# Kernel optimization log

Hardware: AMD Instinct MI355X
Metric: run time of the kernel (lower is better)

Reference implementation:

```python
import jax, jax.numpy as jnp
import numpy as np

EMB = 1024
HEADS = 16
HEAD_DIM = EMB // HEADS
DFF = 4 * EMB
EPS = 1e-5


def setup_inputs() -> dict:
    key = jax.random.key(0)
    ks = jax.random.split(key, 16)
    s = 0.02
    return {
        "x": jax.random.normal(ks[0], (4, 2048, EMB), dtype=jnp.float32),
        "Wq_w": jax.random.normal(ks[1], (EMB, EMB), jnp.float32) * s,
        "Wq_b": jnp.zeros((EMB,), jnp.float32),
        "Wk_w": jax.random.normal(ks[2], (EMB, EMB), jnp.float32) * s,
        "Wk_b": jnp.zeros((EMB,), jnp.float32),
        "Wv_w": jax.random.normal(ks[3], (EMB, EMB), jnp.float32) * s,
        "Wv_b": jnp.zeros((EMB,), jnp.float32),
        "Wo_w": jax.random.normal(ks[4], (EMB, EMB), jnp.float32) * s,
        "Wo_b": jnp.zeros((EMB,), jnp.float32),
        "l1_w": jax.random.normal(ks[5], (DFF, EMB), jnp.float32) * s,
        "l1_b": jnp.zeros((DFF,), jnp.float32),
        "l2_w": jax.random.normal(ks[6], (EMB, DFF), jnp.float32) * s,
        "l2_b": jnp.zeros((EMB,), jnp.float32),
        "n1_scale": jnp.ones((EMB,), jnp.float32),
        "n1_shift": jnp.zeros((EMB,), jnp.float32),
        "n2_scale": jnp.ones((EMB,), jnp.float32),
        "n2_shift": jnp.zeros((EMB,), jnp.float32),
    }


def _layernorm(x, scale, shift):
    # Faithful to the source: mean over last dim, but var over the WHOLE
    # tensor (torch.var with no dim), and divides by var (not std), eps added after.
    mean = jnp.mean(x, axis=-1, keepdims=True)
    var = jnp.var(x)  # scalar, correction=0
    x_norm = (x - mean) / var + EPS
    return x_norm * scale + shift


def _block_forward(x, Wq_w, Wq_b, Wk_w, Wk_b, Wv_w, Wv_b, Wo_w, Wo_b,
                   l1_w, l1_b, l2_w, l2_b, n1_scale, n1_shift, n2_scale, n2_shift):
    B, T, C = x.shape
    shortcut = x
    h = _layernorm(x, n1_scale, n1_shift)

    def proj(w, b):
        y = jnp.einsum('btc,oc->bto', h, w) + b
        return y.reshape(B, T, HEADS, HEAD_DIM).transpose(0, 2, 1, 3)  # bhtd

    q = proj(Wq_w, Wq_b)
    k = proj(Wk_w, Wk_b)
    v = proj(Wv_w, Wv_b)

    scores = jnp.einsum('bhtd,bhsd->bhts', q, k)
    causal = jnp.triu(jnp.ones((T, T), dtype=bool), 1)
    scores = jnp.where(causal, -jnp.inf, scores)
    weights = jax.nn.softmax(scores / jnp.sqrt(jnp.float32(HEAD_DIM)), axis=-1)
    ctx = jnp.einsum('bhts,bhsd->bhtd', weights, v)
    ctx = ctx.transpose(0, 2, 1, 3).reshape(B, T, C)
    attn_out = jnp.einsum('btc,oc->bto', ctx, Wo_w) + Wo_b

    x = attn_out + shortcut
    shortcut = x
    h = _layernorm(x, n2_scale, n2_shift)
    h = jnp.einsum('btc,fc->btf', h, l1_w) + l1_b
    h = jax.nn.gelu(h, approximate=False)
    h = jnp.einsum('btf,cf->btc', h, l2_w) + l2_b
    return h + shortcut


def reference(x, Wq_w, Wq_b, Wk_w, Wk_b, Wv_w, Wv_b, Wo_w, Wo_b,
              l1_w, l1_b, l2_w, l2_b, n1_scale, n1_shift, n2_scale, n2_shift):
    return _block_forward(x, Wq_w, Wq_b, Wk_w, Wk_b, Wv_w, Wv_b, Wo_w, Wo_b,
                          l1_w, l1_b, l2_w, l2_b, n1_scale, n1_shift, n2_scale, n2_shift)
```

## Files before the change

### kernel.cpp

```cpp
#include <hip/hip_runtime.h>
#include <cstdint>

#define EMB   1024
#define HEADS 16
#define HDIM  64
#define DFF   4096
#define TLEN  2048
#define BATCH 4
#define SEQB  8192
#define EPSLN 1e-5f

typedef __attribute__((ext_vector_type(8))) short bf16x8;
typedef __attribute__((ext_vector_type(4))) float f32x4;

#define MFMA16(a, b, c) __builtin_amdgcn_mfma_f32_16x16x32_bf16((a), (b), (c), 0, 0, 0)

__device__ __forceinline__ unsigned short f2bf(float f) {
  unsigned int u = __float_as_uint(f);
  u += 0x7fffu + ((u >> 16) & 1u);
  return (unsigned short)(u >> 16);
}

__device__ __forceinline__ float gelu_f(float x) {
  float x2 = x * x;
  float inner = x * (0.79788456f + 0.035677408f * x2);
  float t = exp2f(2.885390082f * inner);
  return x * t / (t + 1.0f);
}

__global__ __launch_bounds__(256) void cvt_bf16(const float* __restrict__ in,
                                                unsigned short* __restrict__ out, int n4) {
  int i = blockIdx.x * 256 + threadIdx.x;
  if (i >= n4) return;
  float4 v = ((const float4*)in)[i];
  ushort4 o;
  o.x = f2bf(v.x); o.y = f2bf(v.y); o.z = f2bf(v.z); o.w = f2bf(v.w);
  ((ushort4*)out)[i] = o;
}

__global__ __launch_bounds__(256) void pack3(const float* __restrict__ a,
                                             const float* __restrict__ b,
                                             const float* __restrict__ c,
                                             float* __restrict__ o) {
  int i = blockIdx.x * 256 + threadIdx.x;
  o[i] = i < 1024 ? a[i] : (i < 2048 ? b[i - 1024] : c[i - 2048]);
}

__global__ __launch_bounds__(256) void row_reduce(const float* __restrict__ X,
                                                  float* __restrict__ rs,
                                                  float* __restrict__ rq) {
  const int row = blockIdx.x;
  const int tid = threadIdx.x;
  float4 v = ((const float4*)(X + (long)row * EMB))[tid];
  float s = v.x + v.y + v.z + v.w;
  float q = v.x * v.x + v.y * v.y + v.z * v.z + v.w * v.w;
#pragma unroll
  for (int d = 1; d < 64; d <<= 1) { s += __shfl_xor(s, d); q += __shfl_xor(q, d); }
  __shared__ float ss[4], sq[4];
  const int wv = tid >> 6;
  if ((tid & 63) == 0) { ss[wv] = s; sq[wv] = q; }
  __syncthreads();
  if (tid == 0) {
    rs[row] = ss[0] + ss[1] + ss[2] + ss[3];
    rq[row] = sq[0] + sq[1] + sq[2] + sq[3];
  }
}

__global__ __launch_bounds__(256) void finalize_stats(const float* __restrict__ rs,
                                                      const float* __restrict__ rq,
                                                      float* __restrict__ stats) {
  const int tid = threadIdx.x;
  float s = 0.f, q = 0.f;
  for (int i = tid; i < SEQB; i += 256) { s += rs[i]; q += rq[i]; }
#pragma unroll
  for (int d = 1; d < 64; d <<= 1) { s += __shfl_xor(s, d); q += __shfl_xor(q, d); }
  __shared__ float ss[4], sq[4];
  const int wv = tid >> 6;
  if ((tid & 63) == 0) { ss[wv] = s; sq[wv] = q; }
  __syncthreads();
  if (tid == 0) {
    double n = (double)SEQB * (double)EMB;
    double mean = (double)(ss[0] + ss[1] + ss[2] + ss[3]) / n;
    double var = (double)(sq[0] + sq[1] + sq[2] + sq[3]) / n - mean * mean;
    stats[0] = (float)(1.0 / var);
  }
}

__global__ __launch_bounds__(256) void ln_apply(const float* __restrict__ X,
                                                const float* __restrict__ rs,
                                                const float* __restrict__ stats,
                                                const float* __restrict__ scale,
                                                const float* __restrict__ shift,
                                                unsigned short* __restrict__ H) {
  const long i = (long)blockIdx.x * 256 + threadIdx.x;
  const long idx = i * 4;
  const int row = (int)(idx >> 10);
  const int c = (int)(idx & 1023);
  const float mean = rs[row] * (1.0f / EMB);
  const float iv = stats[0];
  float4 x = ((const float4*)X)[i];
  float4 sc = *(const float4*)(scale + c);
  float4 sh = *(const float4*)(shift + c);
  ushort4 o;
  o.x = f2bf(((x.x - mean) * iv + EPSLN) * sc.x + sh.x);
  o.y = f2bf(((x.y - mean) * iv + EPSLN) * sc.y + sh.y);
  o.z = f2bf(((x.z - mean) * iv + EPSLN) * sc.z + sh.z);
  o.w = f2bf(((x.w - mean) * iv + EPSLN) * sc.w + sh.w);
  ((ushort4*)H)[i] = o;
}

template <int EPI>
__global__ __launch_bounds__(256) void gemm_bt(const unsigned short* __restrict__ A,
                                               const unsigned short* __restrict__ W,
                                               const float* __restrict__ bias,
                                               const float* __restrict__ resid,
                                               void* __restrict__ Cout,
                                               unsigned short* __restrict__ kout,
                                               unsigned short* __restrict__ vout,
                                               int M, int N, int K) {
  __shared__ unsigned short sA[128 * 64];
  __shared__ unsigned short sB[128 * 64];
  const int tid = threadIdx.x;
  const int lane = tid & 63;
  const int wave = tid >> 6;
  const int wm = (wave >> 1) * 64, wn = (wave & 1) * 64;
  const int col = lane & 15, quad = lane >> 4;
  const int cx = (col & 7) * 8;

  const int gx = (int)gridDim.x, gy = (int)gridDim.y;
  const int nwg = gx * gy;
  int bid = (int)blockIdx.y * gx + (int)blockIdx.x;
  if ((nwg & 7) == 0) bid = (bid & 7) * (nwg >> 3) + (bid >> 3);
  const int bx = bid % gx;
  const int by = bid / gx;
  const long bm = (long)by * 128, bn = (long)bx * 128;

  f32x4 acc[4][4];
#pragma unroll
  for (int i = 0; i < 4; ++i)
#pragma unroll
    for (int j = 0; j < 4; ++j) acc[i][j] = (f32x4){0.f, 0.f, 0.f, 0.f};

  const int r0 = tid >> 3;
  const int kg = (tid & 7) * 8;
  const int rx = (r0 & 7) * 8;
  const int kgx = kg ^ rx;

  for (int k0 = 0; k0 < K; k0 += 64) {
#pragma unroll
    for (int it = 0; it < 4; ++it) {
      const int r = it * 32 + r0;
      const unsigned short* ga = A + (bm + r) * K + k0 + kgx;
      const unsigned short* gb = W + (bn + r) * K + k0 + kgx;
      __builtin_amdgcn_global_load_lds((const __attribute__((address_space(1))) void*)ga,
                                       (__attribute__((address_space(3))) void*)&sA[r * 64 + kg],
                                       16, 0, 0);
      __builtin_amdgcn_global_load_lds((const __attribute__((address_space(1))) void*)gb,
                                       (__attribute__((address_space(3))) void*)&sB[r * 64 + kg],
                                       16, 0, 0);
    }
    __syncthreads();
#pragma unroll
    for (int ks = 0; ks < 2; ++ks) {
      const int off = (ks * 32 + quad * 8) ^ cx;
      bf16x8 af[4], bfr[4];
#pragma unroll
      for (int mt = 0; mt < 4; ++mt)
        af[mt] = *(const bf16x8*)&sA[(wm + mt * 16 + col) * 64 + off];
#pragma unroll
      for (int nt = 0; nt < 4; ++nt)
        bfr[nt] = *(const bf16x8*)&sB[(wn + nt * 16 + col) * 64 + off];
#pragma unroll
      for (int mt = 0; mt < 4; ++mt)
#pragma unroll
        for (int nt = 0; nt < 4; ++nt) acc[mt][nt] = MFMA16(af[mt], bfr[nt], acc[mt][nt]);
    }
    __syncthreads();
  }

#pragma unroll
  for (int mt = 0; mt < 4; ++mt) {
    const long row0 = bm + wm + mt * 16 + quad * 4;
#pragma unroll
    for (int nt = 0; nt < 4; ++nt) {
      const long c = bn + wn + nt * 16 + col;
      const float bv = bias[c];
      if (EPI == 4) {
        const int seg = (int)(bn >> 10);
        if (seg == 2) {
          ushort4 o;
#pragma unroll
          for (int r = 0; r < 4; ++r) o[r] = f2bf(acc[mt][nt][r] + bv);
          const long bidx = row0 >> 11;
          const long t0 = row0 & 2047;
          *(ushort4*)(vout + (((bidx * 1024 + (c & 1023)) << 11) + t0)) = o;
        } else {
          unsigned short* dst = seg == 0 ? (unsigned short*)Cout : kout;
#pragma unroll
          for (int r = 0; r < 4; ++r)
            dst[(row0 + r) * 1024 + (c & 1023)] = f2bf(acc[mt][nt][r] + bv);
        }
      } else {
#pragma unroll
        for (int r = 0; r < 4; ++r) {
          const long row = row0 + r;
          float v = acc[mt][nt][r] + bv;
          if (EPI == 0) {
            ((unsigned short*)Cout)[row * N + c] = f2bf(v);
          } else if (EPI == 1) {
            ((float*)Cout)[row * N + c] = v + resid[row * N + c];
          } else {
            ((unsigned short*)Cout)[row * N + c] = f2bf(gelu_f(v));
          }
        }
      }
    }
  }
}

#define PSTR 136
__global__ __launch_bounds__(512, 4) void attn7(const unsigned short* __restrict__ Qb,
                                                const unsigned short* __restrict__ Kb,
                                                const unsigned short* __restrict__ vT,
                                                unsigned short* __restrict__ Ctx) {
  __shared__ unsigned short sK[128 * 64];
  __shared__ unsigned short sV[64 * 128];
  __shared__ unsigned short sP[8][16 * PSTR];
  const int bh = blockIdx.x;
  const int pair = blockIdx.y;
  const int b = bh >> 4, h = bh & 15;
  const int tid = threadIdx.x, lane = tid & 63, w = tid >> 6;
  const int col = lane & 15, quad = lane >> 4;
  const int cx = (col & 7) * 8;
  const long bbase = (long)b * TLEN;
  const long hoff = (long)h * HDIM;
  const unsigned short* vbase = vT + (((long)b * 16 + h) * HDIM << 11);
  const float sc2 = 0.125f * 1.44269504088896340736f;

  const int krow = tid >> 3;
  const int kcol = ((tid & 7) * 8) ^ ((krow & 7) * 8);
  const int vrow = tid >> 4;
  const int vcol = ((tid & 15) * 8) ^ ((vrow & 7) * 8);

  for (int phase = 0; phase < 2; ++phase) {
    const int qt = phase == 0 ? (15 - pair) : pair;

    bf16x8 qf[2];
    {
      const long t = (long)qt * 128 + w * 16 + col;
      const unsigned short* qp = Qb + (bbase + t) * EMB + hoff;
#pragma unroll
      for (int ks = 0; ks < 2; ++ks) qf[ks] = *(const bf16x8*)(qp + ks * 32 + quad * 8);
    }

    float li[4] = {0.f, 0.f, 0.f, 0.f};
    f32x4 o[4];
#pragma unroll
    for (int dt = 0; dt < 4; ++dt) o[dt] = (f32x4){0.f, 0.f, 0.f, 0.f};

    for (int kv = 0; kv <= qt; ++kv) {
      __syncthreads();
#pragma unroll
      for (int it = 0; it < 2; ++it) {
        const unsigned short* gk = Kb + (bbase + (long)kv * 128 + it * 64 + krow) * EMB + hoff + kcol;
        __builtin_amdgcn_global_load_lds((const __attribute__((address_space(1))) void*)gk,
                                         (__attribute__((address_space(3))) void*)&sK[it * 4096 + tid * 8],
                                         16, 0, 0);
        const unsigned short* gv = vbase + ((long)(it * 32 + vrow) << 11) + kv * 128 + vcol;
        __builtin_amdgcn_global_load_lds((const __attribute__((address_space(1))) void*)gv,
                                         (__attribute__((address_space(3))) void*)&sV[it * 4096 + tid * 8],
                                         16, 0, 0);
      }
      __syncthreads();

      f32x4 sa[8];
#pragma unroll
      for (int nt = 0; nt < 8; ++nt) sa[nt] = (f32x4){0.f, 0.f, 0.f, 0.f};
#pragma unroll
      for (int ks = 0; ks < 2; ++ks) {
        const int off = (ks * 32 + quad * 8) ^ cx;
#pragma unroll
        for (int nt = 0; nt < 8; ++nt) {
          bf16x8 kf = *(const bf16x8*)&sK[(nt * 16 + col) * 64 + off];
          sa[nt] = MFMA16(qf[ks], kf, sa[nt]);
        }
      }

      if (kv == qt) {
#pragma unroll
        for (int nt = 0; nt < 8; ++nt)
#pragma unroll
          for (int r = 0; r < 4; ++r) {
            const int trel = w * 16 + quad * 4 + r;
            const int srel = nt * 16 + col;
            if (srel > trel) sa[nt][r] = -INFINITY;
          }
      }

#pragma unroll
      for (int nt = 0; nt < 8; ++nt)
#pragma unroll
        for (int r = 0; r < 4; ++r) {
          const float p = exp2f(sa[nt][r] * sc2);
          li[r] += p;
          sP[w][(quad * 4 + r) * PSTR + nt * 16 + col] = f2bf(p);
        }

#pragma unroll
      for (int ks = 0; ks < 4; ++ks) {
        bf16x8 pa = *(const bf16x8*)&sP[w][col * PSTR + ks * 32 + quad * 8];
        const int voff = (ks * 32 + quad * 8) ^ cx;
#pragma unroll
        for (int dt = 0; dt < 4; ++dt) {
          bf16x8 vf = *(const bf16x8*)&sV[(dt * 16 + col) * 128 + voff];
          o[dt] = MFMA16(pa, vf, o[dt]);
        }
      }
    }

#pragma unroll
    for (int d = 1; d < 16; d <<= 1)
#pragma unroll
      for (int r = 0; r < 4; ++r) li[r] += __shfl_xor(li[r], d);
#pragma unroll
    for (int r = 0; r < 4; ++r) {
      const long t = (long)qt * 128 + w * 16 + quad * 4 + r;
      const float inv = 1.0f / li[r];
      unsigned short* cp = Ctx + (bbase + t) * EMB + hoff;
#pragma unroll
      for (int dt = 0; dt < 4; ++dt) cp[dt * 16 + col] = f2bf(o[dt][r] * inv);
    }
  }
}

extern "C" void kernel_launch(void* const* d_in, const int* in_sizes, int n_in,
                              void* d_out, int out_size, void* d_ws, size_t ws_size,
                              hipStream_t stream) {
  const float* x    = (const float*)d_in[0];
  const float* Wq_w = (const float*)d_in[1];
  const float* Wq_b = (const float*)d_in[2];
  const float* Wk_w = (const float*)d_in[3];
  const float* Wk_b = (const float*)d_in[4];
  const float* Wv_w = (const float*)d_in[5];
  const float* Wv_b = (const float*)d_in[6];
  const float* Wo_w = (const float*)d_in[7];
  const float* Wo_b = (const float*)d_in[8];
  const float* l1_w = (const float*)d_in[9];
  const float* l1_b = (const float*)d_in[10];
  const float* l2_w = (const float*)d_in[11];
  const float* l2_b = (const float*)d_in[12];
  const float* n1s  = (const float*)d_in[13];
  const float* n1h  = (const float*)d_in[14];
  const float* n2s  = (const float*)d_in[15];
  const float* n2h  = (const float*)d_in[16];

  char* ws = (char*)d_ws;
  const size_t MB = (size_t)1 << 20;
  unsigned short* wqkv = (unsigned short*)(ws + 0 * MB);
  unsigned short* wo = (unsigned short*)(ws + 6 * MB);
  unsigned short* l1 = (unsigned short*)(ws + 8 * MB);
  unsigned short* l2 = (unsigned short*)(ws + 16 * MB);
  unsigned short* hb = (unsigned short*)(ws + 24 * MB);
  unsigned short* qb = (unsigned short*)(ws + 40 * MB);
  unsigned short* kb = (unsigned short*)(ws + 56 * MB);
  unsigned short* vb = (unsigned short*)(ws + 72 * MB);
  unsigned short* cb = (unsigned short*)(ws + 88 * MB);
  unsigned short* gb = qb;
  float* x2 = (float*)(ws + 104 * MB);
  float* rs = (float*)(ws + 136 * MB);
  float* rq = (float*)(ws + 136 * MB + 64 * 1024);
  float* st = (float*)(ws + 136 * MB + 128 * 1024);
  float* bqkv = (float*)(ws + 136 * MB + 192 * 1024);

  cvt_bf16<<<1024, 256, 0, stream>>>(Wq_w, wqkv, EMB * EMB / 4);
  cvt_bf16<<<1024, 256, 0, stream>>>(Wk_w, wqkv + 1024 * 1024, EMB * EMB / 4);
  cvt_bf16<<<1024, 256, 0, stream>>>(Wv_w, wqkv + 2048 * 1024, EMB * EMB / 4);
  cvt_bf16<<<1024, 256, 0, stream>>>(Wo_w, wo, EMB * EMB / 4);
  cvt_bf16<<<4096, 256, 0, stream>>>(l1_w, l1, DFF * EMB / 4);
  cvt_bf16<<<4096, 256, 0, stream>>>(l2_w, l2, EMB * DFF / 4);
  pack3<<<12, 256, 0, stream>>>(Wq_b, Wk_b, Wv_b, bqkv);

  row_reduce<<<SEQB, 256, 0, stream>>>(x, rs, rq);
  finalize_stats<<<1, 256, 0, stream>>>(rs, rq, st);
  ln_apply<<<SEQB, 256, 0, stream>>>(x, rs, st, n1s, n1h, hb);

  dim3 g1(EMB / 128, SEQB / 128);
  gemm_bt<4><<<dim3(3 * EMB / 128, SEQB / 128), 256, 0, stream>>>(
      hb, wqkv, bqkv, nullptr, qb, kb, vb, SEQB, 3 * EMB, EMB);

  attn7<<<dim3(BATCH * HEADS, 8), 512, 0, stream>>>(qb, kb, vb, cb);

  gemm_bt<1><<<g1, 256, 0, stream>>>(cb, wo, Wo_b, x, (void*)x2, nullptr, nullptr, SEQB, EMB, EMB);

  row_reduce<<<SEQB, 256, 0, stream>>>(x2, rs, rq);
  finalize_stats<<<1, 256, 0, stream>>>(rs, rq, st);
  ln_apply<<<SEQB, 256, 0, stream>>>(x2, rs, st, n2s, n2h, hb);

  gemm_bt<2><<<dim3(DFF / 128, SEQB / 128), 256, 0, stream>>>(hb, l1, l1_b, nullptr, gb, nullptr, nullptr, SEQB, DFF, EMB);
  gemm_bt<1><<<g1, 256, 0, stream>>>(gb, l2, l2_b, x2, d_out, nullptr, nullptr, SEQB, EMB, DFF);
}
```

Measured before the change: 552.3 us.

## Replace GEMM with 256x256-tile, 8-wave, double-buffered LDS pipelined kernel

Replaces the 128x128 single-buffered GEMM with a 256x256-tile kernel using 512 threads (8 waves, each 128x64). Global-to-LDS loads for the next K step are split into quarter stages interleaved with MFMA phases. Explicit vmcnt waits, barriers and setprio let loads overlap compute. The LDS layout is reswizzled for 32-wide K halves. This targets global-load latency and raises reuse per loaded byte, but uses more LDS and registers, which lowers occupancy, and the grid has fewer blocks.

```diff
diff --git a/kernel.cpp b/kernel.cpp
--- a/kernel.cpp
+++ b/kernel.cpp
@@ -109,77 +109,135 @@
   ((ushort4*)H)[i] = o;
 }
 
+#define STAGE_HALF(GSRC, LDST)                                                              \
+  do {                                                                                      \
+    _Pragma("unroll") for (int j_ = 0; j_ < 2; ++j_) {                                      \
+      __builtin_amdgcn_global_load_lds(                                                     \
+          (const __attribute__((address_space(1))) void*)((GSRC) +                          \
+                                                          (long)(j_ * 128 + (tid >> 2)) * K), \
+          (__attribute__((address_space(3))) void*)((LDST) + j_ * 4096 + tid * 8), 16, 0, 0); \
+    }                                                                                       \
+  } while (0)
+
 template <int EPI>
-__global__ __launch_bounds__(256) void gemm_bt(const unsigned short* __restrict__ A,
-                                               const unsigned short* __restrict__ W,
-                                               const float* __restrict__ bias,
-                                               const float* __restrict__ resid,
-                                               void* __restrict__ Cout,
-                                               unsigned short* __restrict__ kout,
-                                               unsigned short* __restrict__ vout,
-                                               int M, int N, int K) {
-  __shared__ unsigned short sA[128 * 64];
-  __shared__ unsigned short sB[128 * 64];
+__global__ __launch_bounds__(512, 2) void gemm8(const unsigned short* __restrict__ A,
+                                                const unsigned short* __restrict__ W,
+                                                const float* __restrict__ bias,
+                                                const float* __restrict__ resid,
+                                                void* __restrict__ Cout,
+                                                unsigned short* __restrict__ kout,
+                                                unsigned short* __restrict__ vout,
+                                                int M, int N, int K) {
+  __shared__ unsigned short lds[2][2][2][8192];
   const int tid = threadIdx.x;
   const int lane = tid & 63;
   const int wave = tid >> 6;
-  const int wm = (wave >> 1) * 64, wn = (wave & 1) * 64;
+  const int wm = (wave >> 2) * 128, wn = (wave & 3) * 64;
   const int col = lane & 15, quad = lane >> 4;
-  const int cx = (col & 7) * 8;
+  const int rq8 = (quad ^ ((col >> 1) & 3)) * 8;
+  const int scol = ((tid & 3) ^ ((tid >> 3) & 3)) * 8;
 
   const int gx = (int)gridDim.x, gy = (int)gridDim.y;
   const int nwg = gx * gy;
   int bid = (int)blockIdx.y * gx + (int)blockIdx.x;
   if ((nwg & 7) == 0) bid = (bid & 7) * (nwg >> 3) + (bid >> 3);
-  const int bx = bid % gx;
-  const int by = bid / gx;
-  const long bm = (long)by * 128, bn = (long)bx * 128;
-
-  f32x4 acc[4][4];
-#pragma unroll
-  for (int i = 0; i < 4; ++i)
+  const long bm = (long)(bid / gx) * 256, bn = (long)(bid % gx) * 256;
+
+  const unsigned short* Abase = A + bm * K;
+  const unsigned short* Bbase = W + bn * K;
+
+  f32x4 acc[8][4];
+#pragma unroll
+  for (int i = 0; i < 8; ++i)
 #pragma unroll
     for (int j = 0; j < 4; ++j) acc[i][j] = (f32x4){0.f, 0.f, 0.f, 0.f};
 
-  const int r0 = tid >> 3;
-  const int kg = (tid & 7) * 8;
-  const int rx = (r0 & 7) * 8;
-  const int kgx = kg ^ rx;
-
-  for (int k0 = 0; k0 < K; k0 += 64) {
-#pragma unroll
-    for (int it = 0; it < 4; ++it) {
-      const int r = it * 32 + r0;
-      const unsigned short* ga = A + (bm + r) * K + k0 + kgx;
-      const unsigned short* gb = W + (bn + r) * K + k0 + kgx;
-      __builtin_amdgcn_global_load_lds((const __attribute__((address_space(1))) void*)ga,
-                                       (__attribute__((address_space(3))) void*)&sA[r * 64 + kg],
-                                       16, 0, 0);
-      __builtin_amdgcn_global_load_lds((const __attribute__((address_space(1))) void*)gb,
-                                       (__attribute__((address_space(3))) void*)&sB[r * 64 + kg],
-                                       16, 0, 0);
-    }
-    __syncthreads();
-#pragma unroll
-    for (int ks = 0; ks < 2; ++ks) {
-      const int off = (ks * 32 + quad * 8) ^ cx;
-      bf16x8 af[4], bfr[4];
-#pragma unroll
-      for (int mt = 0; mt < 4; ++mt)
-        af[mt] = *(const bf16x8*)&sA[(wm + mt * 16 + col) * 64 + off];
-#pragma unroll
-      for (int nt = 0; nt < 4; ++nt)
-        bfr[nt] = *(const bf16x8*)&sB[(wn + nt * 16 + col) * 64 + off];
-#pragma unroll
-      for (int mt = 0; mt < 4; ++mt)
-#pragma unroll
-        for (int nt = 0; nt < 4; ++nt) acc[mt][nt] = MFMA16(af[mt], bfr[nt], acc[mt][nt]);
-    }
-    __syncthreads();
+  STAGE_HALF(Abase + scol, &lds[0][0][0][0]);
+  STAGE_HALF(Bbase + scol, &lds[0][1][0][0]);
+  STAGE_HALF(Abase + 32 + scol, &lds[0][0][1][0]);
+  STAGE_HALF(Bbase + 32 + scol, &lds[0][1][1][0]);
+
+  const int nk = K >> 6;
+  for (int t = 0; t < nk; ++t) {
+    const int c = t & 1;
+    const bool pf = (t + 1) < nk;
+    const long koff = (long)(t + 1) * 64;
+    unsigned short* sAc = &lds[c][0][0][0];
+    unsigned short* sBc = &lds[c][1][0][0];
+    unsigned short* sAn = &lds[c ^ 1][0][0][0];
+    unsigned short* sBn = &lds[c ^ 1][1][0][0];
+    bf16x8 af[4], bfr[4];
+
+    asm volatile("s_waitcnt vmcnt(4)" ::: "memory");
+    __builtin_amdgcn_sched_barrier(0);
+    __builtin_amdgcn_s_barrier();
+    asm volatile("" ::: "memory");
+    if (pf) STAGE_HALF(Abase + koff + scol, sAn);
+#pragma unroll
+    for (int nt = 0; nt < 4; ++nt) bfr[nt] = *(const bf16x8*)&sBc[(wn + nt * 16 + col) * 32 + rq8];
+#pragma unroll
+    for (int mt = 0; mt < 4; ++mt) af[mt] = *(const bf16x8*)&sAc[(wm + mt * 16 + col) * 32 + rq8];
+    asm volatile("s_waitcnt lgkmcnt(0)" ::: "memory");
+    __builtin_amdgcn_sched_barrier(0);
+    __builtin_amdgcn_s_setprio(1);
+#pragma unroll
+    for (int mt = 0; mt < 4; ++mt)
+#pragma unroll
+      for (int nt = 0; nt < 4; ++nt) acc[mt][nt] = MFMA16(af[mt], bfr[nt], acc[mt][nt]);
+    __builtin_amdgcn_s_setprio(0);
+
+    __builtin_amdgcn_sched_barrier(0);
+    __builtin_amdgcn_s_barrier();
+    asm volatile("" ::: "memory");
+    if (pf) STAGE_HALF(Bbase + koff + scol, sBn);
+#pragma unroll
+    for (int mt = 0; mt < 4; ++mt) af[mt] = *(const bf16x8*)&sAc[(wm + (mt + 4) * 16 + col) * 32 + rq8];
+    asm volatile("s_waitcnt lgkmcnt(0)" ::: "memory");
+    __builtin_amdgcn_sched_barrier(0);
+    __builtin_amdgcn_s_setprio(1);
+#pragma unroll
+    for (int mt = 0; mt < 4; ++mt)
+#pragma unroll
+      for (int nt = 0; nt < 4; ++nt) acc[mt + 4][nt] = MFMA16(af[mt], bfr[nt], acc[mt + 4][nt]);
+    __builtin_amdgcn_s_setprio(0);
+
+    if (pf) asm volatile("s_waitcnt vmcnt(4)" ::: "memory");
+    else    asm volatile("s_waitcnt vmcnt(0)" ::: "memory");
+    __builtin_amdgcn_sched_barrier(0);
+    __builtin_amdgcn_s_barrier();
+    asm volatile("" ::: "memory");
+    if (pf) STAGE_HALF(Abase + koff + 32 + scol, sAn + 8192);
+#pragma unroll
+    for (int nt = 0; nt < 4; ++nt) bfr[nt] = *(const bf16x8*)&sBc[8192 + (wn + nt * 16 + col) * 32 + rq8];
+#pragma unroll
+    for (int mt = 0; mt < 4; ++mt) af[mt] = *(const bf16x8*)&sAc[8192 + (wm + mt * 16 + col) * 32 + rq8];
+    asm volatile("s_waitcnt lgkmcnt(0)" ::: "memory");
+    __builtin_amdgcn_sched_barrier(0);
+    __builtin_amdgcn_s_setprio(1);
+#pragma unroll
+    for (int mt = 0; mt < 4; ++mt)
+#pragma unroll
+      for (int nt = 0; nt < 4; ++nt) acc[mt][nt] = MFMA16(af[mt], bfr[nt], acc[mt][nt]);
+    __builtin_amdgcn_s_setprio(0);
+
+    __builtin_amdgcn_sched_barrier(0);
+    __builtin_amdgcn_s_barrier();
+    asm volatile("" ::: "memory");
+    if (pf) STAGE_HALF(Bbase + koff + 32 + scol, sBn + 8192);
+#pragma unroll
+    for (int mt = 0; mt < 4; ++mt) af[mt] = *(const bf16x8*)&sAc[8192 + (wm + (mt + 4) * 16 + col) * 32 + rq8];
+    asm volatile("s_waitcnt lgkmcnt(0)" ::: "memory");
+    __builtin_amdgcn_sched_barrier(0);
+    __builtin_amdgcn_s_setprio(1);
+#pragma unroll
+    for (int mt = 0; mt < 4; ++mt)
+#pragma unroll
+      for (int nt = 0; nt < 4; ++nt) acc[mt + 4][nt] = MFMA16(af[mt], bfr[nt], acc[mt + 4][nt]);
+    __builtin_amdgcn_s_setprio(0);
   }
 
 #pragma unroll
-  for (int mt = 0; mt < 4; ++mt) {
+  for (int mt = 0; mt < 8; ++mt) {
     const long row0 = bm + wm + mt * 16 + quad * 4;
 #pragma unroll
     for (int nt = 0; nt < 4; ++nt) {
@@ -205,9 +263,7 @@
         for (int r = 0; r < 4; ++r) {
           const long row = row0 + r;
           float v = acc[mt][nt][r] + bv;
-          if (EPI == 0) {
-            ((unsigned short*)Cout)[row * N + c] = f2bf(v);
-          } else if (EPI == 1) {
+          if (EPI == 1) {
             ((float*)Cout)[row * N + c] = v + resid[row * N + c];
           } else {
             ((unsigned short*)Cout)[row * N + c] = f2bf(gelu_f(v));
@@ -384,18 +440,18 @@
   finalize_stats<<<1, 256, 0, stream>>>(rs, rq, st);
   ln_apply<<<SEQB, 256, 0, stream>>>(x, rs, st, n1s, n1h, hb);
 
-  dim3 g1(EMB / 128, SEQB / 128);
-  gemm_bt<4><<<dim3(3 * EMB / 128, SEQB / 128), 256, 0, stream>>>(
+  dim3 g256(EMB / 256, SEQB / 256);
+  gemm8<4><<<dim3(3 * EMB / 256, SEQB / 256), 512, 0, stream>>>(
       hb, wqkv, bqkv, nullptr, qb, kb, vb, SEQB, 3 * EMB, EMB);
 
   attn7<<<dim3(BATCH * HEADS, 8), 512, 0, stream>>>(qb, kb, vb, cb);
 
-  gemm_bt<1><<<g1, 256, 0, stream>>>(cb, wo, Wo_b, x, (void*)x2, nullptr, nullptr, SEQB, EMB, EMB);
+  gemm8<1><<<g256, 512, 0, stream>>>(cb, wo, Wo_b, x, (void*)x2, nullptr, nullptr, SEQB, EMB, EMB);
 
   row_reduce<<<SEQB, 256, 0, stream>>>(x2, rs, rq);
   finalize_stats<<<1, 256, 0, stream>>>(rs, rq, st);
   ln_apply<<<SEQB, 256, 0, stream>>>(x2, rs, st, n2s, n2h, hb);
 
-  gemm_bt<2><<<dim3(DFF / 128, SEQB / 128), 256, 0, stream>>>(hb, l1, l1_b, nullptr, gb, nullptr, nullptr, SEQB, DFF, EMB);
-  gemm_bt<1><<<g1, 256, 0, stream>>>(gb, l2, l2_b, x2, d_out, nullptr, nullptr, SEQB, EMB, DFF);
-}
+  gemm8<2><<<dim3(DFF / 256, SEQB / 256), 512, 0, stream>>>(hb, l1, l1_b, nullptr, gb, nullptr, nullptr, SEQB, DFF, EMB);
+  gemm8<1><<<g256, 512, 0, stream>>>(gb, l2, l2_b, x2, d_out, nullptr, nullptr, SEQB, EMB, DFF);
+}
```

Measured after the change: 594.6 us. 1.08x slower.
